# Kernel optimization log

Measured on AMD Instinct MI355X. Metric: run time of the kernel, lower is better.

## Reference

```python
import jax, jax.numpy as jnp
import numpy as np

DIM = 512
HEADS = 8
DIM_HEAD = 64
BLOCK_SIZE = 2048
B, N = 4, 2048
EPS = 1e-5


def setup_inputs() -> dict:
    key = jax.random.key(0)
    ks = jax.random.split(key, 8)
    hd = HEADS * DIM_HEAD
    std = 0.02
    return {
        "x": jax.random.normal(ks[0], (B, N, DIM), dtype=jnp.float32),
        "ln_w": jnp.ones((DIM,), jnp.float32),
        "ln_b": jnp.zeros((DIM,), jnp.float32),
        # linear weights stored [in, out]
        "wq": jax.random.normal(ks[1], (DIM, hd), jnp.float32) * std,
        "wk": jax.random.normal(ks[2], (DIM, hd), jnp.float32) * std,
        "wv": jax.random.normal(ks[3], (DIM, hd), jnp.float32) * std,
        "bv": jnp.zeros((hd,), jnp.float32),
        "wo": jax.random.normal(ks[4], (hd, DIM), jnp.float32) * std,
        "bo": jnp.zeros((DIM,), jnp.float32),
        "pe": jax.random.normal(ks[5], (1, BLOCK_SIZE, DIM), jnp.float32) * std,
    }


def reference(x, ln_w, ln_b, wq, wk, wv, bv, wo, bo, pe):
    # x: [b, n, dim] (channel_last=True path)
    b, n, _ = x.shape
    x_in = x
    # LayerNorm over last dim
    mu = jnp.mean(x, axis=-1, keepdims=True)
    var = jnp.var(x, axis=-1, keepdims=True)
    h = (x - mu) * jax.lax.rsqrt(var + EPS) * ln_w + ln_b
    # positional embedding
    h = h + pe[:, :n]
    # QKV projections -> [b, heads, n, dim_head]
    def split_heads(t):
        return t.reshape(b, n, HEADS, DIM_HEAD).transpose(0, 2, 1, 3)
    q = split_heads(h @ wq)
    k = split_heads(h @ wk)
    v = split_heads(h @ wv + bv)
    # attention
    scale = float(DIM_HEAD) ** -0.5
    attn = jnp.einsum('bhid,bhjd->bhij', q, k) * scale
    attn = jax.nn.softmax(attn, axis=-1)
    out = jnp.einsum('bhij,bhjd->bhid', attn, v)
    out = out.transpose(0, 2, 1, 3).reshape(b, n, HEADS * DIM_HEAD)
    out = out @ wo + bo
    return x_in + out
```

## Files before the change

kernel.cpp:

```cpp
#include <hip/hip_runtime.h>


typedef __bf16 bf16;
typedef __bf16 bf16x2 __attribute__((ext_vector_type(2)));
typedef __bf16 bf16x4 __attribute__((ext_vector_type(4)));
typedef __bf16 bf16x8 __attribute__((ext_vector_type(8)));
typedef float  f32x4  __attribute__((ext_vector_type(4)));

#define MFMA16(a, b, c) __builtin_amdgcn_mfma_f32_16x16x32_bf16((a), (b), (c), 0, 0, 0)

#if __has_builtin(__builtin_amdgcn_exp2f)
#define EXP2(x) __builtin_amdgcn_exp2f(x)
#else
#define EXP2(x) exp2f(x)
#endif

__device__ __forceinline__ void gload16(const void* g, void* l) {
  __builtin_amdgcn_global_load_lds(
      (const __attribute__((address_space(1))) unsigned int*)g,
      (__attribute__((address_space(3))) unsigned int*)l, 16, 0, 0);
}

__global__ void wtrans_kernel(const float* __restrict__ wq, const float* __restrict__ wk,
                              const float* __restrict__ wv, const float* __restrict__ wo,
                              bf16* __restrict__ wqkvT, bf16* __restrict__ woT) {
  __shared__ float tile[32][33];
  int z = blockIdx.z;
  const float* src = (z == 0) ? wq : (z == 1) ? wk : (z == 2) ? wv : wo;
  bf16* dst = (z < 3) ? (wqkvT + (size_t)z * 512 * 512) : woT;
  int bx = blockIdx.x, by = blockIdx.y;
  int tx = threadIdx.x, ty = threadIdx.y;
#pragma unroll
  for (int yy = 0; yy < 4; ++yy)
    tile[ty + 8 * yy][tx] = src[(size_t)(by * 32 + ty + 8 * yy) * 512 + bx * 32 + tx];
  __syncthreads();
#pragma unroll
  for (int yy = 0; yy < 4; ++yy)
    dst[(size_t)(bx * 32 + ty + 8 * yy) * 512 + by * 32 + tx] = (bf16)tile[tx][ty + 8 * yy];
}

__global__ __launch_bounds__(256) void ln_pe_kernel(const float* __restrict__ x,
                                                    const float* __restrict__ w,
                                                    const float* __restrict__ b,
                                                    const float* __restrict__ pe,
                                                    bf16* __restrict__ h) {
  const int row = blockIdx.x * 4 + (threadIdx.x >> 6);
  const int lane = threadIdx.x & 63;
  const float4* xr = (const float4*)(x + (size_t)row * 512) + lane * 2;
  const float4 a = xr[0], c = xr[1];
  float s = a.x + a.y + a.z + a.w + c.x + c.y + c.z + c.w;
  float ss = a.x * a.x + a.y * a.y + a.z * a.z + a.w * a.w +
             c.x * c.x + c.y * c.y + c.z * c.z + c.w * c.w;
#pragma unroll
  for (int off = 1; off <= 32; off <<= 1) {
    s += __shfl_xor(s, off);
    ss += __shfl_xor(ss, off);
  }
  const float mu = s * (1.0f / 512.0f);
  const float var = ss * (1.0f / 512.0f) - mu * mu;
  const float rs = rsqrtf(var + 1e-5f);
  const float4* wr = (const float4*)w + lane * 2;
  const float4* br = (const float4*)b + lane * 2;
  const float4* pr = (const float4*)(pe + (size_t)(row & 2047) * 512) + lane * 2;
  const float4 w0 = wr[0], w1 = wr[1], b0 = br[0], b1 = br[1], p0 = pr[0], p1 = pr[1];
  bf16x8 o;
  o[0] = (bf16)((a.x - mu) * rs * w0.x + b0.x + p0.x);
  o[1] = (bf16)((a.y - mu) * rs * w0.y + b0.y + p0.y);
  o[2] = (bf16)((a.z - mu) * rs * w0.z + b0.z + p0.z);
  o[3] = (bf16)((a.w - mu) * rs * w0.w + b0.w + p0.w);
  o[4] = (bf16)((c.x - mu) * rs * w1.x + b1.x + p1.x);
  o[5] = (bf16)((c.y - mu) * rs * w1.y + b1.y + p1.y);
  o[6] = (bf16)((c.z - mu) * rs * w1.z + b1.z + p1.z);
  o[7] = (bf16)((c.w - mu) * rs * w1.w + b1.w + p1.w);
  *(bf16x8*)(h + (size_t)row * 512 + lane * 8) = o;
}

__device__ __forceinline__ void gemm_tile(const bf16* __restrict__ A,
                                          const bf16* __restrict__ Bt,
                                          f32x4 acc[4][4]) {
  __shared__ char lds[32768];
  const int tid = threadIdx.x, wave = tid >> 6, lane = tid & 63;
  const int wrow = wave >> 1, wcol = wave & 1;
  const int l15 = lane & 15, lg = lane >> 4;
  const char* Ab = (const char*)A + (size_t)blockIdx.x * 128 * 1024;
  const char* Bb = (const char*)Bt + (size_t)blockIdx.y * 128 * 1024;
  const int r0 = wave * 32 + (lane >> 2);
  const int cb = (lane & 3) * 16;
  const size_t so = (size_t)r0 * 1024 + cb;

  const f32x4 z = {0.f, 0.f, 0.f, 0.f};
#pragma unroll
  for (int mi = 0; mi < 4; ++mi)
#pragma unroll
    for (int ni = 0; ni < 4; ++ni) acc[mi][ni] = z;

  {
    char* nb = lds;
    gload16(Ab + so, nb + wave * 2048);
    gload16(Ab + so + 16 * 1024, nb + wave * 2048 + 1024);
    gload16(Bb + so, nb + 8192 + wave * 2048);
    gload16(Bb + so + 16 * 1024, nb + 8192 + wave * 2048 + 1024);
  }
  __syncthreads();

  for (int kt = 0; kt < 16; ++kt) {
    if (kt < 15) {
      char* nb = lds + ((kt + 1) & 1) * 16384;
      const char* As = Ab + so + (kt + 1) * 64;
      const char* Bs = Bb + so + (kt + 1) * 64;
      gload16(As, nb + wave * 2048);
      gload16(As + 16 * 1024, nb + wave * 2048 + 1024);
      gload16(Bs, nb + 8192 + wave * 2048);
      gload16(Bs + 16 * 1024, nb + 8192 + wave * 2048 + 1024);
    }
    char* lA = lds + (kt & 1) * 16384;
    char* lB = lA + 8192;
    bf16x8 av[4], bv[4];
#pragma unroll
    for (int mi = 0; mi < 4; ++mi)
      av[mi] = *(const bf16x8*)(lA + (wrow * 64 + mi * 16 + l15) * 64 + lg * 16);
#pragma unroll
    for (int ni = 0; ni < 4; ++ni)
      bv[ni] = *(const bf16x8*)(lB + (wcol * 64 + ni * 16 + l15) * 64 + lg * 16);
    __builtin_amdgcn_s_setprio(1);
#pragma unroll
    for (int mi = 0; mi < 4; ++mi)
#pragma unroll
      for (int ni = 0; ni < 4; ++ni)
        acc[mi][ni] = MFMA16(av[mi], bv[ni], acc[mi][ni]);
    __builtin_amdgcn_s_setprio(0);
    __syncthreads();
  }
}

__global__ __launch_bounds__(256, 3) void gemm_qkv_kernel(
    const bf16* __restrict__ h, const bf16* __restrict__ wqkvT,
    const float* __restrict__ bvec, bf16* __restrict__ qo, bf16* __restrict__ ko,
    bf16* __restrict__ vo) {
  f32x4 acc[4][4];
  gemm_tile(h, wqkvT, acc);
  const int tid = threadIdx.x, wave = tid >> 6, lane = tid & 63;
  const int wrow = wave >> 1, wcol = wave & 1;
  const int l15 = lane & 15, lg = lane >> 4;
  const int row0 = blockIdx.x * 128 + wrow * 64;
  const int col0 = blockIdx.y * 128 + wcol * 64;
#pragma unroll
  for (int mi = 0; mi < 4; ++mi) {
#pragma unroll
    for (int ni = 0; ni < 4; ++ni) {
      int c = col0 + ni * 16 + l15;
      int proj = c >> 9;
      int wc = c & 511;
      int head = wc >> 6, d = wc & 63;
      int rb = row0 + mi * 16 + lg * 4;
      int bb = rb >> 11, n = rb & 2047;
      if (proj == 2) {
        float bias = bvec[wc];
        bf16x4 pv;
#pragma unroll
        for (int reg = 0; reg < 4; ++reg) pv[reg] = (bf16)(acc[mi][ni][reg] + bias);
        *(bf16x4*)(vo + ((size_t)(bb * 8 + head) * 64 + d) * 2048 + n) = pv;
      } else if (proj == 0) {
#pragma unroll
        for (int reg = 0; reg < 4; ++reg)
          qo[((size_t)(bb * 8 + head) * 2048 + (n + reg)) * 64 + d] =
              (bf16)(acc[mi][ni][reg] * (0.125f * 1.44269504f));
      } else {
#pragma unroll
        for (int reg = 0; reg < 4; ++reg)
          ko[((size_t)(bb * 8 + head) * 2048 + (n + reg)) * 64 + d] =
              (bf16)acc[mi][ni][reg];
      }
    }
  }
}

__global__ __launch_bounds__(256, 4) void attn_kernel(const bf16* __restrict__ q,
                                                      const bf16* __restrict__ k,
                                                      const bf16* __restrict__ v,
                                                      bf16* __restrict__ ao) {
  __shared__ char lds[40960];
  const int tid = threadIdx.x, wave = tid >> 6, lane = tid & 63;
  const int l15 = lane & 15, lg = lane >> 4;
  const int swzr = (l15 & 7) << 4;

  const int bid = blockIdx.x;
  const int xcd = bid & 7, slot = bid >> 3;
  const int bh = xcd + 8 * (slot >> 5);
  const int qt = slot & 31;
  const int bb = bh >> 3, hh = bh & 7;

  const char* ksrc = (const char*)(k + (size_t)bh * 2048 * 64);
  const char* vsrc = (const char*)(v + (size_t)bh * 64 * 2048);
  const int r0 = wave * 16 + (lane >> 3);
  const int colb = (lane & 7) * 16;
  const size_t ko0 = (size_t)r0 * 128 + (colb ^ ((r0 & 7) << 4));
  const size_t vo0 = (size_t)r0 * 4096 + (colb ^ ((r0 & 7) << 4));
  char* Pw = lds + 32768 + wave * 2048;

  const bf16* qbase = q + ((size_t)bh * 2048 + qt * 64 + wave * 16) * 64;
  bf16x8 qf[2];
#pragma unroll
  for (int dk = 0; dk < 2; ++dk)
    qf[dk] = *(const bf16x8*)(qbase + l15 * 64 + dk * 32 + lg * 8);

  const f32x4 z = {0.f, 0.f, 0.f, 0.f};
  f32x4 oacc[4] = {z, z, z, z};
  float mrun = -1e30f, lrun = 0.f;

  gload16(ksrc + ko0, lds + wave * 2048);
  gload16(ksrc + ko0 + 1024, lds + wave * 2048 + 1024);
  gload16(vsrc + vo0, lds + 8192 + wave * 2048);
  gload16(vsrc + vo0 + 8 * 4096, lds + 8192 + wave * 2048 + 1024);
  __syncthreads();

  for (int t = 0; t < 32; ++t) {
    if (t + 1 < 32) {
      char* nb = lds + ((t + 1) & 1) * 16384;
      const char* ks = ksrc + (size_t)(t + 1) * 8192 + ko0;
      const char* vs = vsrc + (size_t)(t + 1) * 128 + vo0;
      gload16(ks, nb + wave * 2048);
      gload16(ks + 1024, nb + wave * 2048 + 1024);
      gload16(vs, nb + 8192 + wave * 2048);
      gload16(vs + 8 * 4096, nb + 8192 + wave * 2048 + 1024);
    }
    char* Ksh = lds + (t & 1) * 16384;
    char* Vsh = Ksh + 8192;

    __builtin_amdgcn_s_setprio(1);
    bf16x8 kf[4][2];
#pragma unroll
    for (int kt = 0; kt < 4; ++kt)
#pragma unroll
      for (int dk = 0; dk < 2; ++dk)
        kf[kt][dk] = *(const bf16x8*)(Ksh + (kt * 16 + l15) * 128 +
                                      ((dk * 64 + lg * 16) ^ swzr));
    f32x4 sacc[4] = {z, z, z, z};
#pragma unroll
    for (int dk = 0; dk < 2; ++dk)
#pragma unroll
      for (int kt = 0; kt < 4; ++kt)
        sacc[kt] = MFMA16(kf[kt][dk], qf[dk], sacc[kt]);
    __builtin_amdgcn_s_setprio(0);

    float mt = fmaxf(fmaxf(sacc[0][0], sacc[0][1]), fmaxf(sacc[0][2], sacc[0][3]));
#pragma unroll
    for (int kt = 1; kt < 4; ++kt)
      mt = fmaxf(mt, fmaxf(fmaxf(sacc[kt][0], sacc[kt][1]),
                           fmaxf(sacc[kt][2], sacc[kt][3])));
    mt = fmaxf(mt, __shfl_xor(mt, 16));
    mt = fmaxf(mt, __shfl_xor(mt, 32));
    if (__any(mt > mrun + 11.5f)) {
      float mn = fmaxf(mrun, mt);
      float sc = EXP2(mrun - mn);
      mrun = mn;
      lrun *= sc;
      float scr[4];
#pragma unroll
      for (int reg = 0; reg < 4; ++reg) scr[reg] = __shfl(sc, lg * 4 + reg);
#pragma unroll
      for (int ds = 0; ds < 4; ++ds)
#pragma unroll
        for (int reg = 0; reg < 4; ++reg) oacc[ds][reg] *= scr[reg];
    }
    float rs = 0.f;
#pragma unroll
    for (int kt = 0; kt < 4; ++kt) {
      bf16x4 pv;
#pragma unroll
      for (int reg = 0; reg < 4; ++reg) {
        float p = EXP2(sacc[kt][reg] - mrun);
        pv[reg] = (bf16)p;
        rs += p;
      }
      *(bf16x4*)(Pw + l15 * 128 + ((kt * 32 + lg * 8) ^ swzr)) = pv;
    }
    rs += __shfl_xor(rs, 16);
    rs += __shfl_xor(rs, 32);
    lrun += rs;

    __builtin_amdgcn_s_setprio(1);
#pragma unroll
    for (int ks = 0; ks < 2; ++ks) {
      bf16x8 pf = *(const bf16x8*)(Pw + l15 * 128 + ((ks * 64 + lg * 16) ^ swzr));
#pragma unroll
      for (int ds = 0; ds < 4; ++ds) {
        bf16x8 vf = *(const bf16x8*)(Vsh + (ds * 16 + l15) * 128 +
                                     ((ks * 64 + lg * 16) ^ swzr));
        oacc[ds] = MFMA16(pf, vf, oacc[ds]);
      }
    }
    __builtin_amdgcn_s_setprio(0);
    __syncthreads();
  }

  const int qrow0 = qt * 64 + wave * 16;
#if __has_builtin(__builtin_amdgcn_rcpf)
  float rin = __builtin_amdgcn_rcpf(lrun);
#else
  float rin = 1.0f / lrun;
#endif
  float rr[4];
#pragma unroll
  for (int reg = 0; reg < 4; ++reg) rr[reg] = __shfl(rin, lg * 4 + reg);
#pragma unroll
  for (int ds = 0; ds < 4; ++ds)
#pragma unroll
    for (int reg = 0; reg < 4; ++reg) {
      int n = qrow0 + lg * 4 + reg;
      ao[((size_t)bb * 2048 + n) * 512 + hh * 64 + ds * 16 + l15] =
          (bf16)(oacc[ds][reg] * rr[reg]);
    }
}

__global__ __launch_bounds__(256, 3) void gemm_out_kernel(
    const bf16* __restrict__ ao, const bf16* __restrict__ woT,
    const float* __restrict__ bo, const float* __restrict__ x,
    float* __restrict__ out) {
  f32x4 acc[4][4];
  gemm_tile(ao, woT, acc);
  const int tid = threadIdx.x, wave = tid >> 6, lane = tid & 63;
  const int wrow = wave >> 1, wcol = wave & 1;
  const int l15 = lane & 15, lg = lane >> 4;
  const int row0 = blockIdx.x * 128 + wrow * 64;
  const int col0 = blockIdx.y * 128 + wcol * 64;
#pragma unroll
  for (int mi = 0; mi < 4; ++mi) {
#pragma unroll
    for (int ni = 0; ni < 4; ++ni) {
      int c = col0 + ni * 16 + l15;
      float bias = bo[c];
#pragma unroll
      for (int reg = 0; reg < 4; ++reg) {
        int r = row0 + mi * 16 + lg * 4 + reg;
        size_t ofs = (size_t)r * 512 + c;
        out[ofs] = acc[mi][ni][reg] + bias + x[ofs];
      }
    }
  }
}

extern "C" void kernel_launch(void* const* d_in, const int* in_sizes, int n_in,
                              void* d_out, int out_size, void* d_ws, size_t ws_size,
                              hipStream_t stream) {
  const float* x   = (const float*)d_in[0];
  const float* lnw = (const float*)d_in[1];
  const float* lnb = (const float*)d_in[2];
  const float* wq  = (const float*)d_in[3];
  const float* wk  = (const float*)d_in[4];
  const float* wv  = (const float*)d_in[5];
  const float* bv  = (const float*)d_in[6];
  const float* wo  = (const float*)d_in[7];
  const float* bo  = (const float*)d_in[8];
  const float* pe  = (const float*)d_in[9];
  float* out = (float*)d_out;

  char* ws = (char*)d_ws;
  bf16* hbuf  = (bf16*)(ws);
  bf16* wqkvT = (bf16*)(ws + 8388608);
  bf16* woT   = (bf16*)(ws + 9961472);
  bf16* qb    = (bf16*)(ws + 10485760);
  bf16* kb    = (bf16*)(ws + 18874368);
  bf16* vb    = (bf16*)(ws + 27262976);
  bf16* aob   = hbuf;

  hipLaunchKernelGGL(wtrans_kernel, dim3(16, 16, 4), dim3(32, 8), 0, stream,
                     wq, wk, wv, wo, wqkvT, woT);
  hipLaunchKernelGGL(ln_pe_kernel, dim3(2048), dim3(256), 0, stream,
                     x, lnw, lnb, pe, hbuf);
  hipLaunchKernelGGL(gemm_qkv_kernel, dim3(64, 12), dim3(256), 0, stream,
                     hbuf, wqkvT, bv, qb, kb, vb);
  hipLaunchKernelGGL(attn_kernel, dim3(1024), dim3(256), 0, stream,
                     qb, kb, vb, aob);
  hipLaunchKernelGGL(gemm_out_kernel, dim3(64, 4), dim3(256), 0, stream,
                     aob, woT, bo, x, out);
}
```

Before: 179.5 us.

## Rewrite attention with 32x32 MFMA, register-resident P, and larger tiles

The attention kernel moves from 16x16x32 to 32x32x16 bf16 MFMA. Each block now covers 128 queries (32 per wave) and each step loads 128 keys into a 64KB double buffer, so the grid is halved. The P tile no longer goes through LDS: probabilities are packed with v_cvt_pk_bf16 and rearranged across lanes with v_permlane32_swap into the operand layout the MFMA expects. This removes LDS round trips and raises MFMA work per load, at the cost of lower occupancy (launch bounds 2, larger LDS) and higher register pressure.

```diff
diff --git a/kernel.cpp b/kernel.cpp
--- a/kernel.cpp
+++ b/kernel.cpp
@@ -6,8 +6,12 @@
 typedef __bf16 bf16x4 __attribute__((ext_vector_type(4)));
 typedef __bf16 bf16x8 __attribute__((ext_vector_type(8)));
 typedef float  f32x4  __attribute__((ext_vector_type(4)));
+typedef float  f32x16 __attribute__((ext_vector_type(16)));
+typedef unsigned int u32;
+typedef u32 u32x4 __attribute__((ext_vector_type(4)));
 
 #define MFMA16(a, b, c) __builtin_amdgcn_mfma_f32_16x16x32_bf16((a), (b), (c), 0, 0, 0)
+#define MFMA32(a, b, c) __builtin_amdgcn_mfma_f32_32x32x16_bf16((a), (b), (c), 0, 0, 0)
 
 #if __has_builtin(__builtin_amdgcn_exp2f)
 #define EXP2(x) __builtin_amdgcn_exp2f(x)
@@ -19,6 +23,15 @@
   __builtin_amdgcn_global_load_lds(
       (const __attribute__((address_space(1))) unsigned int*)g,
       (__attribute__((address_space(3))) unsigned int*)l, 16, 0, 0);
+}
+
+__device__ __forceinline__ u32 cvt_pk_bf16(float lo, float hi) {
+  u32 r;
+  asm("v_cvt_pk_bf16_f32 %0, %1, %2" : "=v"(r) : "v"(lo), "v"(hi));
+  return r;
+}
+__device__ __forceinline__ void permswap(u32& a, u32& b) {
+  asm volatile("v_permlane32_swap_b32 %0, %1" : "+v"(a), "+v"(b));
 }
 
 __global__ void wtrans_kernel(const float* __restrict__ wq, const float* __restrict__ wk,
@@ -175,142 +188,158 @@
   }
 }
 
-__global__ __launch_bounds__(256, 4) void attn_kernel(const bf16* __restrict__ q,
+__global__ __launch_bounds__(256, 2) void attn_kernel(const bf16* __restrict__ q,
                                                       const bf16* __restrict__ k,
                                                       const bf16* __restrict__ v,
                                                       bf16* __restrict__ ao) {
-  __shared__ char lds[40960];
+  __shared__ char lds[65536];
   const int tid = threadIdx.x, wave = tid >> 6, lane = tid & 63;
-  const int l15 = lane & 15, lg = lane >> 4;
-  const int swzr = (l15 & 7) << 4;
+  const int l31 = lane & 31, hi = lane >> 5;
 
   const int bid = blockIdx.x;
   const int xcd = bid & 7, slot = bid >> 3;
-  const int bh = xcd + 8 * (slot >> 5);
-  const int qt = slot & 31;
+  const int bh = xcd + 8 * (slot >> 4);
+  const int qt = slot & 15;
   const int bb = bh >> 3, hh = bh & 7;
 
   const char* ksrc = (const char*)(k + (size_t)bh * 2048 * 64);
   const char* vsrc = (const char*)(v + (size_t)bh * 64 * 2048);
-  const int r0 = wave * 16 + (lane >> 3);
-  const int colb = (lane & 7) * 16;
-  const size_t ko0 = (size_t)r0 * 128 + (colb ^ ((r0 & 7) << 4));
-  const size_t vo0 = (size_t)r0 * 4096 + (colb ^ ((r0 & 7) << 4));
-  char* Pw = lds + 32768 + wave * 2048;
-
-  const bf16* qbase = q + ((size_t)bh * 2048 + qt * 64 + wave * 16) * 64;
-  bf16x8 qf[2];
-#pragma unroll
-  for (int dk = 0; dk < 2; ++dk)
-    qf[dk] = *(const bf16x8*)(qbase + l15 * 64 + dk * 32 + lg * 8);
-
-  const f32x4 z = {0.f, 0.f, 0.f, 0.f};
-  f32x4 oacc[4] = {z, z, z, z};
+
+  const int krow0 = wave * 32 + (lane >> 3);
+  const int kcolb = (lane & 7) * 16;
+  const int vrow0 = wave * 16 + (lane >> 4);
+  const int vcolb = (lane & 15) * 16;
+
+  const int q0 = qt * 128 + wave * 32;
+  const bf16* qbase = q + ((size_t)bh * 2048 + q0) * 64;
+  bf16x8 qf[4];
+#pragma unroll
+  for (int ks = 0; ks < 4; ++ks)
+    qf[ks] = *(const bf16x8*)(qbase + l31 * 64 + ks * 16 + hi * 8);
+
+  f32x16 oacc[2] = {};
   float mrun = -1e30f, lrun = 0.f;
 
-  gload16(ksrc + ko0, lds + wave * 2048);
-  gload16(ksrc + ko0 + 1024, lds + wave * 2048 + 1024);
-  gload16(vsrc + vo0, lds + 8192 + wave * 2048);
-  gload16(vsrc + vo0 + 8 * 4096, lds + 8192 + wave * 2048 + 1024);
+#define STAGE(T, BUF)                                                          \
+  {                                                                            \
+    char* Kd = (BUF);                                                          \
+    char* Vd = (BUF) + 16384;                                                  \
+    const char* kg = ksrc + (size_t)(T) * 16384;                               \
+    const char* vg = vsrc + (size_t)(T) * 256;                                 \
+    _Pragma("unroll") for (int i = 0; i < 4; ++i) {                            \
+      int r = krow0 + i * 8;                                                   \
+      gload16(kg + (size_t)r * 128 + (kcolb ^ ((r & 7) << 4)),                 \
+              Kd + (wave * 32 + i * 8) * 128);                                 \
+      int rv = vrow0 + i * 4;                                                  \
+      gload16(vg + (size_t)rv * 4096 + (vcolb ^ ((rv & 15) << 4)),             \
+              Vd + (wave * 16 + i * 4) * 256);                                 \
+    }                                                                          \
+  }
+
+  STAGE(0, lds);
   __syncthreads();
 
-  for (int t = 0; t < 32; ++t) {
-    if (t + 1 < 32) {
-      char* nb = lds + ((t + 1) & 1) * 16384;
-      const char* ks = ksrc + (size_t)(t + 1) * 8192 + ko0;
-      const char* vs = vsrc + (size_t)(t + 1) * 128 + vo0;
-      gload16(ks, nb + wave * 2048);
-      gload16(ks + 1024, nb + wave * 2048 + 1024);
-      gload16(vs, nb + 8192 + wave * 2048);
-      gload16(vs + 8 * 4096, nb + 8192 + wave * 2048 + 1024);
+  for (int t = 0; t < 16; ++t) {
+    if (t + 1 < 16) STAGE(t + 1, lds + ((t + 1) & 1) * 32768);
+    char* Ksh = lds + (t & 1) * 32768;
+    char* Vsh = Ksh + 16384;
+
+#pragma unroll
+    for (int sub = 0; sub < 2; ++sub) {
+      f32x16 sacc[2] = {};
+      __builtin_amdgcn_s_setprio(1);
+#pragma unroll
+      for (int kt = 0; kt < 2; ++kt) {
+        const int row = sub * 64 + kt * 32 + l31;
+        const int swz = (row & 7) << 4;
+#pragma unroll
+        for (int ks = 0; ks < 4; ++ks) {
+          bf16x8 kf = *(const bf16x8*)(Ksh + row * 128 + ((ks * 32 + hi * 16) ^ swz));
+          sacc[kt] = MFMA32(kf, qf[ks], sacc[kt]);
+        }
+      }
+      __builtin_amdgcn_s_setprio(0);
+
+      float mt = sacc[0][0];
+#pragma unroll
+      for (int kt = 0; kt < 2; ++kt)
+#pragma unroll
+        for (int reg = 0; reg < 16; ++reg) mt = fmaxf(mt, sacc[kt][reg]);
+      mt = fmaxf(mt, __shfl_xor(mt, 32));
+      if (__any(mt > mrun + 11.5f)) {
+        float mn = fmaxf(mrun, mt);
+        float sc = EXP2(mrun - mn);
+        mrun = mn;
+        lrun *= sc;
+#pragma unroll
+        for (int reg = 0; reg < 16; ++reg) {
+          float s2 = __shfl(sc, (reg & 3) + 8 * (reg >> 2) + 4 * hi);
+          oacc[0][reg] *= s2;
+          oacc[1][reg] *= s2;
+        }
+      }
+      float rs = 0.f;
+      u32 c[2][8];
+#pragma unroll
+      for (int kt = 0; kt < 2; ++kt)
+#pragma unroll
+        for (int gp = 0; gp < 4; ++gp) {
+          float p0 = EXP2(sacc[kt][gp * 4 + 0] - mrun);
+          float p1 = EXP2(sacc[kt][gp * 4 + 1] - mrun);
+          float p2 = EXP2(sacc[kt][gp * 4 + 2] - mrun);
+          float p3 = EXP2(sacc[kt][gp * 4 + 3] - mrun);
+          rs += (p0 + p1) + (p2 + p3);
+          c[kt][gp * 2 + 0] = cvt_pk_bf16(p0, p1);
+          c[kt][gp * 2 + 1] = cvt_pk_bf16(p2, p3);
+        }
+      lrun += rs;
+
+      bf16x8 pf[4];
+#pragma unroll
+      for (int kt = 0; kt < 2; ++kt)
+#pragma unroll
+        for (int mm = 0; mm < 2; ++mm) {
+          u32 a0 = c[kt][mm * 4 + 0], b0 = c[kt][mm * 4 + 2];
+          u32 a1 = c[kt][mm * 4 + 1], b1 = c[kt][mm * 4 + 3];
+          permswap(a0, b0);
+          permswap(a1, b1);
+          union { u32x4 w; bf16x8 v; } u;
+          u.w = (u32x4){a0, a1, b0, b1};
+          pf[kt * 2 + mm] = u.v;
+        }
+
+      __builtin_amdgcn_s_setprio(1);
+#pragma unroll
+      for (int dt = 0; dt < 2; ++dt) {
+        const int row = dt * 32 + l31;
+        const int swz = (row & 15) << 4;
+#pragma unroll
+        for (int m = 0; m < 4; ++m) {
+          bf16x8 vf = *(const bf16x8*)(Vsh + row * 256 +
+                                       ((sub * 128 + m * 32 + hi * 16) ^ swz));
+          oacc[dt] = MFMA32(pf[m], vf, oacc[dt]);
+        }
+      }
+      __builtin_amdgcn_s_setprio(0);
     }
-    char* Ksh = lds + (t & 1) * 16384;
-    char* Vsh = Ksh + 8192;
-
-    __builtin_amdgcn_s_setprio(1);
-    bf16x8 kf[4][2];
-#pragma unroll
-    for (int kt = 0; kt < 4; ++kt)
-#pragma unroll
-      for (int dk = 0; dk < 2; ++dk)
-        kf[kt][dk] = *(const bf16x8*)(Ksh + (kt * 16 + l15) * 128 +
-                                      ((dk * 64 + lg * 16) ^ swzr));
-    f32x4 sacc[4] = {z, z, z, z};
-#pragma unroll
-    for (int dk = 0; dk < 2; ++dk)
-#pragma unroll
-      for (int kt = 0; kt < 4; ++kt)
-        sacc[kt] = MFMA16(kf[kt][dk], qf[dk], sacc[kt]);
-    __builtin_amdgcn_s_setprio(0);
-
-    float mt = fmaxf(fmaxf(sacc[0][0], sacc[0][1]), fmaxf(sacc[0][2], sacc[0][3]));
-#pragma unroll
-    for (int kt = 1; kt < 4; ++kt)
-      mt = fmaxf(mt, fmaxf(fmaxf(sacc[kt][0], sacc[kt][1]),
-                           fmaxf(sacc[kt][2], sacc[kt][3])));
-    mt = fmaxf(mt, __shfl_xor(mt, 16));
-    mt = fmaxf(mt, __shfl_xor(mt, 32));
-    if (__any(mt > mrun + 11.5f)) {
-      float mn = fmaxf(mrun, mt);
-      float sc = EXP2(mrun - mn);
-      mrun = mn;
-      lrun *= sc;
-      float scr[4];
-#pragma unroll
-      for (int reg = 0; reg < 4; ++reg) scr[reg] = __shfl(sc, lg * 4 + reg);
-#pragma unroll
-      for (int ds = 0; ds < 4; ++ds)
-#pragma unroll
-        for (int reg = 0; reg < 4; ++reg) oacc[ds][reg] *= scr[reg];
-    }
-    float rs = 0.f;
-#pragma unroll
-    for (int kt = 0; kt < 4; ++kt) {
-      bf16x4 pv;
-#pragma unroll
-      for (int reg = 0; reg < 4; ++reg) {
-        float p = EXP2(sacc[kt][reg] - mrun);
-        pv[reg] = (bf16)p;
-        rs += p;
-      }
-      *(bf16x4*)(Pw + l15 * 128 + ((kt * 32 + lg * 8) ^ swzr)) = pv;
-    }
-    rs += __shfl_xor(rs, 16);
-    rs += __shfl_xor(rs, 32);
-    lrun += rs;
-
-    __builtin_amdgcn_s_setprio(1);
-#pragma unroll
-    for (int ks = 0; ks < 2; ++ks) {
-      bf16x8 pf = *(const bf16x8*)(Pw + l15 * 128 + ((ks * 64 + lg * 16) ^ swzr));
-#pragma unroll
-      for (int ds = 0; ds < 4; ++ds) {
-        bf16x8 vf = *(const bf16x8*)(Vsh + (ds * 16 + l15) * 128 +
-                                     ((ks * 64 + lg * 16) ^ swzr));
-        oacc[ds] = MFMA16(pf, vf, oacc[ds]);
-      }
-    }
-    __builtin_amdgcn_s_setprio(0);
     __syncthreads();
   }
-
-  const int qrow0 = qt * 64 + wave * 16;
+#undef STAGE
+
+  lrun += __shfl_xor(lrun, 32);
 #if __has_builtin(__builtin_amdgcn_rcpf)
   float rin = __builtin_amdgcn_rcpf(lrun);
 #else
   float rin = 1.0f / lrun;
 #endif
-  float rr[4];
-#pragma unroll
-  for (int reg = 0; reg < 4; ++reg) rr[reg] = __shfl(rin, lg * 4 + reg);
-#pragma unroll
-  for (int ds = 0; ds < 4; ++ds)
-#pragma unroll
-    for (int reg = 0; reg < 4; ++reg) {
-      int n = qrow0 + lg * 4 + reg;
-      ao[((size_t)bb * 2048 + n) * 512 + hh * 64 + ds * 16 + l15] =
-          (bf16)(oacc[ds][reg] * rr[reg]);
-    }
+#pragma unroll
+  for (int reg = 0; reg < 16; ++reg) {
+    int qrow = (reg & 3) + 8 * (reg >> 2) + 4 * hi;
+    float rr = __shfl(rin, qrow);
+    size_t base = ((size_t)bb * 2048 + q0 + qrow) * 512 + hh * 64;
+    ao[base + l31] = (bf16)(oacc[0][reg] * rr);
+    ao[base + 32 + l31] = (bf16)(oacc[1][reg] * rr);
+  }
 }
 
 __global__ __launch_bounds__(256, 3) void gemm_out_kernel(
@@ -370,7 +399,7 @@
                      x, lnw, lnb, pe, hbuf);
   hipLaunchKernelGGL(gemm_qkv_kernel, dim3(64, 12), dim3(256), 0, stream,
                      hbuf, wqkvT, bv, qb, kb, vb);
-  hipLaunchKernelGGL(attn_kernel, dim3(1024), dim3(256), 0, stream,
+  hipLaunchKernelGGL(attn_kernel, dim3(512), dim3(256), 0, stream,
                      qb, kb, vb, aob);
   hipLaunchKernelGGL(gemm_out_kernel, dim3(64, 4), dim3(256), 0, stream,
                      aob, woT, bo, x, out);
```

After: 169.7 us. -5.4%, faster.
